# Optimization experiments

Hardware: AMD Instinct MI355X
Metric: run time of the kernel (lower is better)

## Reference

```python
import jax, jax.numpy as jnp
import numpy as np
from jax import lax

DSTATE, DINPUT, DMLP1, DMLP2, TRAJ = 64, 4, 256, 256, 8
BATCH, SEQ = 1024, 64


def setup_inputs() -> dict:
    key = jax.random.key(0)
    ks = jax.random.split(key, 4)
    f32 = jnp.float32
    return {
        "quat_seq": jax.random.normal(ks[0], (BATCH, SEQ, DINPUT), f32),
        "W1": jax.random.normal(ks[1], (DSTATE + DINPUT, DMLP1), f32) / np.sqrt(DSTATE + DINPUT),
        "b1": jnp.zeros((DMLP1,), f32),
        "W2": jax.random.normal(ks[2], (DMLP1, DMLP2), f32) / np.sqrt(DMLP1),
        "b2": jnp.zeros((DMLP2,), f32),
        "W3": jax.random.normal(ks[3], (DMLP2, DSTATE), f32) / np.sqrt(DMLP2),
        "b3": jnp.zeros((DSTATE,), f32),
    }


def reference(quat_seq, W1, b1, W2, b2, W3, b3):
    dt = 1.0 / (TRAJ - 1)  # uniform linspace(0,1,TRAJ) step

    def odefunc(h, q):
        # 3-layer tanh MLP on concat([h, q]); time-independent
        x = jnp.concatenate([h, q], axis=-1)          # [B, dstate+dinput]
        h1 = jnp.tanh(x @ W1 + b1)
        h2 = jnp.tanh(h1 @ W2 + b2)
        return h2 @ W3 + b3                            # [B, dstate]

    @jax.checkpoint
    def rk4_step(h, q):
        # torchdiffeq 'rk4' uses the 3/8-rule variant (rk4_alt_step_func)
        k1 = odefunc(h, q)
        k2 = odefunc(h + dt * k1 / 3.0, q)
        k3 = odefunc(h + dt * (k2 - k1 / 3.0), q)
        k4 = odefunc(h + dt * (k1 - k2 + k3), q)
        return h + dt * (k1 + 3.0 * (k2 + k3) + k4) / 8.0

    def per_token(h, q):
        # integrate over t_span, recording TRAJ states (including initial h)
        def body(hc, _):
            hn = rk4_step(hc, q)
            return hn, hn
        h_last, tail = lax.scan(body, h, None, length=TRAJ - 1)
        h_traj = jnp.concatenate([h[None], tail], axis=0)  # [TRAJ, B, dstate]
        return h_last, h_traj

    B = quat_seq.shape[0]
    h0 = jnp.zeros((B, DSTATE), quat_seq.dtype).at[:, 0].set(1.0)
    qs = jnp.swapaxes(quat_seq, 0, 1)  # [seq, B, dinput]
    h_final, trajs = lax.scan(per_token, h0, qs)  # trajs: [seq, TRAJ, B, dstate]
    trajectories = jnp.transpose(trajs, (2, 0, 1, 3))  # [B, seq, TRAJ, dstate]
    return h_final, trajectories
```

## Files before the change

kernel.cpp:

```cpp
#include <hip/hip_runtime.h>
#include <math.h>

#define NTHR 512
#define BT 4

__device__ __forceinline__ float fast_tanh(float x) {
    float ax = fabsf(x);
    float e  = __expf(-2.0f * ax);
    float r  = (1.0f - e) * __builtin_amdgcn_rcpf(1.0f + e);
    return copysignf(r, x);
}

__global__ __launch_bounds__(NTHR, 2)
void odernn_kernel(const float* __restrict__ quat,
                   const float* __restrict__ W1,
                   const float* __restrict__ b1,
                   const float* __restrict__ W2,
                   const float* __restrict__ b2,
                   const float* __restrict__ W3,
                   const float* __restrict__ b3,
                   float* __restrict__ out)
{
    __shared__ __align__(16) float sRed[8192];
    __shared__ __align__(16) float sH1[4][256];
    __shared__ __align__(16) float sH2[4][256];
    __shared__ __align__(16) float sC1[4][256];
    __shared__ __align__(16) float sY[4][64];

    const int t = threadIdx.x;
    const int w = t >> 6;
    const int l = t & 63;
    const int b0 = blockIdx.x * BT;

    const int j1a = t >> 1;
    const int kha = (t & 1) * 32;
    const int kb2 = w * 32;
    const int j1c = t & 255;
    const int bc  = (t >> 8) * 2;
    const int u3  = t & 15;
    const int ks3 = t >> 4;
    const int kb3 = ks3 * 8;
    const int rb = w;
    const int rj = l;

    float w1r[32];
    #pragma unroll
    for (int k = 0; k < 32; ++k) w1r[k] = W1[(kha + k) * 256 + j1a];

    float w2r[128];
    const float4* __restrict__ W2v4 = (const float4*)W2;
    #pragma unroll
    for (int k = 0; k < 32; ++k) {
        float4 v = W2v4[(size_t)(kb2 + k) * 64 + l];
        w2r[k * 4 + 0] = v.x; w2r[k * 4 + 1] = v.y;
        w2r[k * 4 + 2] = v.z; w2r[k * 4 + 3] = v.w;
    }
    float w3r[32];
    #pragma unroll
    for (int k = 0; k < 8; ++k) {
        float4 v = *(const float4*)&W3[(kb3 + k) * 64 + u3 * 4];
        w3r[k * 4 + 0] = v.x; w3r[k * 4 + 1] = v.y;
        w3r[k * 4 + 2] = v.z; w3r[k * 4 + 3] = v.w;
    }
    float w1q[4];
    #pragma unroll
    for (int m = 0; m < 4; ++m) w1q[m] = W1[(64 + m) * 256 + j1c];

    const float rb1  = b1[j1c];
    const float rb2c = b2[j1c];
    const float rb3e = b3[rj];

    float rH  = (rj == 0) ? 1.0f : 0.0f;
    float rk1 = 0.0f, rk2 = 0.0f, rk3 = 0.0f;
    if (t < 256) sY[rb][rj] = rH;

    const float dt = 1.0f / 7.0f;
    float* __restrict__ traj = out + 1024 * 64;

    for (int s = 0; s < 64; ++s) {
        if (t < 256) {
            float4 q0 = *(const float4*)&quat[((size_t)(b0 + 0) * 64 + s) * 4];
            float4 q1 = *(const float4*)&quat[((size_t)(b0 + 1) * 64 + s) * 4];
            float4 q2 = *(const float4*)&quat[((size_t)(b0 + 2) * 64 + s) * 4];
            float4 q3 = *(const float4*)&quat[((size_t)(b0 + 3) * 64 + s) * 4];
            sC1[0][t] = fmaf(q0.x, w1q[0], fmaf(q0.y, w1q[1], fmaf(q0.z, w1q[2], fmaf(q0.w, w1q[3], rb1))));
            sC1[1][t] = fmaf(q1.x, w1q[0], fmaf(q1.y, w1q[1], fmaf(q1.z, w1q[2], fmaf(q1.w, w1q[3], rb1))));
            sC1[2][t] = fmaf(q2.x, w1q[0], fmaf(q2.y, w1q[1], fmaf(q2.z, w1q[2], fmaf(q2.w, w1q[3], rb1))));
            sC1[3][t] = fmaf(q3.x, w1q[0], fmaf(q3.y, w1q[1], fmaf(q3.z, w1q[2], fmaf(q3.w, w1q[3], rb1))));
            traj[(((size_t)(b0 + rb) * 64 + s) * 8 + 0) * 64 + rj] = rH;
        }
        __syncthreads();

        for (int step = 1; step < 8; ++step) {
            #pragma unroll
            for (int mode = 1; mode <= 4; ++mode) {
                {
                    float a0 = 0.0f, a1 = 0.0f, a2 = 0.0f, a3 = 0.0f;
                    const float4* y4 = (const float4*)&sY[0][0];
                    const int yb = (t & 1) * 8;
                    #pragma unroll
                    for (int k4 = 0; k4 < 8; ++k4) {
                        float4 y0 = y4[0 * 16 + yb + k4];
                        float4 y1 = y4[1 * 16 + yb + k4];
                        float4 y2 = y4[2 * 16 + yb + k4];
                        float4 y3 = y4[3 * 16 + yb + k4];
                        #pragma unroll
                        for (int r = 0; r < 4; ++r) {
                            float wv = w1r[k4 * 4 + r];
                            a0 = fmaf(((const float*)&y0)[r], wv, a0);
                            a1 = fmaf(((const float*)&y1)[r], wv, a1);
                            a2 = fmaf(((const float*)&y2)[r], wv, a2);
                            a3 = fmaf(((const float*)&y3)[r], wv, a3);
                        }
                    }
                    a0 += __shfl_xor(a0, 1);
                    a1 += __shfl_xor(a1, 1);
                    a2 += __shfl_xor(a2, 1);
                    a3 += __shfl_xor(a3, 1);
                    const int bw = (t & 1) * 2;
                    float vA = (t & 1) ? a2 : a0;
                    float vB = (t & 1) ? a3 : a1;
                    sH1[bw][j1a]     = fast_tanh(vA + sC1[bw][j1a]);
                    sH1[bw + 1][j1a] = fast_tanh(vB + sC1[bw + 1][j1a]);
                }
                __syncthreads();
                {
                    float acc[4][4];
                    #pragma unroll
                    for (int bb = 0; bb < 4; ++bb)
                        #pragma unroll
                        for (int jj = 0; jj < 4; ++jj) acc[bb][jj] = 0.0f;
                    #pragma unroll
                    for (int k4 = 0; k4 < 8; ++k4) {
                        const int k = kb2 + k4 * 4;
                        float4 h0 = *(const float4*)&sH1[0][k];
                        float4 h1v = *(const float4*)&sH1[1][k];
                        float4 h2v = *(const float4*)&sH1[2][k];
                        float4 h3v = *(const float4*)&sH1[3][k];
                        #pragma unroll
                        for (int r = 0; r < 4; ++r) {
                            const int wi = (k4 * 4 + r) * 4;
                            float f0 = ((const float*)&h0)[r];
                            float f1 = ((const float*)&h1v)[r];
                            float f2 = ((const float*)&h2v)[r];
                            float f3 = ((const float*)&h3v)[r];
                            #pragma unroll
                            for (int jj = 0; jj < 4; ++jj) {
                                acc[0][jj] = fmaf(f0, w2r[wi + jj], acc[0][jj]);
                                acc[1][jj] = fmaf(f1, w2r[wi + jj], acc[1][jj]);
                                acc[2][jj] = fmaf(f2, w2r[wi + jj], acc[2][jj]);
                                acc[3][jj] = fmaf(f3, w2r[wi + jj], acc[3][jj]);
                            }
                        }
                    }
                    #pragma unroll
                    for (int bb = 0; bb < 4; ++bb)
                        *(float4*)&sRed[w * 1024 + bb * 256 + l * 4] =
                            make_float4(acc[bb][0], acc[bb][1], acc[bb][2], acc[bb][3]);
                }
                __syncthreads();
                {
                    float v0 = rb2c, v1 = 0.0f, u0 = rb2c, u1 = 0.0f;
                    #pragma unroll
                    for (int ks = 0; ks < 8; ks += 2) {
                        v0 += sRed[ks * 1024 + bc * 256 + j1c];
                        u0 += sRed[ks * 1024 + (bc + 1) * 256 + j1c];
                        v1 += sRed[(ks + 1) * 1024 + bc * 256 + j1c];
                        u1 += sRed[(ks + 1) * 1024 + (bc + 1) * 256 + j1c];
                    }
                    sH2[bc][j1c]     = fast_tanh(v0 + v1);
                    sH2[bc + 1][j1c] = fast_tanh(u0 + u1);
                }
                __syncthreads();
                {
                    float acc[4][4];
                    #pragma unroll
                    for (int bb = 0; bb < 4; ++bb)
                        #pragma unroll
                        for (int jj = 0; jj < 4; ++jj) acc[bb][jj] = 0.0f;
                    #pragma unroll
                    for (int k4 = 0; k4 < 2; ++k4) {
                        const int k = kb3 + k4 * 4;
                        float4 h0 = *(const float4*)&sH2[0][k];
                        float4 h1v = *(const float4*)&sH2[1][k];
                        float4 h2v = *(const float4*)&sH2[2][k];
                        float4 h3v = *(const float4*)&sH2[3][k];
                        #pragma unroll
                        for (int r = 0; r < 4; ++r) {
                            const int wi = (k4 * 4 + r) * 4;
                            float f0 = ((const float*)&h0)[r];
                            float f1 = ((const float*)&h1v)[r];
                            float f2 = ((const float*)&h2v)[r];
                            float f3 = ((const float*)&h3v)[r];
                            #pragma unroll
                            for (int jj = 0; jj < 4; ++jj) {
                                acc[0][jj] = fmaf(f0, w3r[wi + jj], acc[0][jj]);
                                acc[1][jj] = fmaf(f1, w3r[wi + jj], acc[1][jj]);
                                acc[2][jj] = fmaf(f2, w3r[wi + jj], acc[2][jj]);
                                acc[3][jj] = fmaf(f3, w3r[wi + jj], acc[3][jj]);
                            }
                        }
                    }
                    #pragma unroll
                    for (int bb = 0; bb < 4; ++bb)
                        *(float4*)&sRed[ks3 * 256 + bb * 64 + u3 * 4] =
                            make_float4(acc[bb][0], acc[bb][1], acc[bb][2], acc[bb][3]);
                }
                __syncthreads();
                if (t < 256) {
                    float s0 = rb3e, s1 = 0.0f, s2 = 0.0f, s3 = 0.0f;
                    #pragma unroll
                    for (int ks = 0; ks < 32; ks += 4) {
                        s0 += sRed[(ks + 0) * 256 + rb * 64 + rj];
                        s1 += sRed[(ks + 1) * 256 + rb * 64 + rj];
                        s2 += sRed[(ks + 2) * 256 + rb * 64 + rj];
                        s3 += sRed[(ks + 3) * 256 + rb * 64 + rj];
                    }
                    float k = (s0 + s1) + (s2 + s3);
                    float ynew;
                    if (mode == 1) {
                        rk1 = k;
                        ynew = fmaf(dt * (1.0f / 3.0f), rk1, rH);
                    } else if (mode == 2) {
                        rk2 = k;
                        ynew = fmaf(dt, rk2 - rk1 * (1.0f / 3.0f), rH);
                    } else if (mode == 3) {
                        rk3 = k;
                        ynew = fmaf(dt, rk1 - rk2 + rk3, rH);
                    } else {
                        rH = fmaf(dt * 0.125f, rk1 + 3.0f * (rk2 + rk3) + k, rH);
                        ynew = rH;
                        traj[(((size_t)(b0 + rb) * 64 + s) * 8 + step) * 64 + rj] = rH;
                    }
                    sY[rb][rj] = ynew;
                }
                __syncthreads();
            }
        }
    }
    if (t < 256) out[(size_t)(b0 + rb) * 64 + rj] = rH;
}

extern "C" void kernel_launch(void* const* d_in, const int* in_sizes, int n_in,
                              void* d_out, int out_size, void* d_ws, size_t ws_size,
                              hipStream_t stream) {
    const float* quat = (const float*)d_in[0];
    const float* W1   = (const float*)d_in[1];
    const float* b1   = (const float*)d_in[2];
    const float* W2   = (const float*)d_in[3];
    const float* b2   = (const float*)d_in[4];
    const float* W3   = (const float*)d_in[5];
    const float* b3   = (const float*)d_in[6];
    float* out = (float*)d_out;

    odernn_kernel<<<1024 / BT, NTHR, 0, stream>>>(quat, W1, b1, W2, b2, W3, b3, out);
}
```

Measured before the change: 5.657 ms.

## Replace shared-memory split-K reductions with in-wave shuffle reductions

Layers 2 and 3 change their work split so that the K-slices for each output column live in lanes of the same wavefront. The partial sums are then reduced with xor-shuffles instead of being written to a shared-memory scratch buffer and summed after an extra barrier. This removes the 32 KB sRed buffer and two __syncthreads per RK stage. The layer-1 q-projection weights are now reloaded from global memory every token to free registers. K-offsets are rotated per lane to avoid LDS bank conflicts. The cost is many more shuffle instructions and some duplicated work across lanes.

```diff
diff --git a/kernel.cpp b/kernel.cpp
--- a/kernel.cpp
+++ b/kernel.cpp
@@ -21,7 +21,6 @@
                    const float* __restrict__ b3,
                    float* __restrict__ out)
 {
-    __shared__ __align__(16) float sRed[8192];
     __shared__ __align__(16) float sH1[4][256];
     __shared__ __align__(16) float sH2[4][256];
     __shared__ __align__(16) float sC1[4][256];
@@ -33,62 +32,79 @@
     const int b0 = blockIdx.x * BT;
 
     const int j1a = t >> 1;
-    const int kha = (t & 1) * 32;
-    const int kb2 = w * 32;
-    const int j1c = t & 255;
-    const int bc  = (t >> 8) * 2;
-    const int u3  = t & 15;
-    const int ks3 = t >> 4;
-    const int kb3 = ks3 * 8;
-    const int rb = w;
-    const int rj = l;
+    const int bw  = (t & 1) * 2;
+    const int yb  = (t & 1) * 8;
+    const int ks2 = l & 7;
+    const int u2  = (w << 3) | (l >> 3);
+    const int kb2 = ks2 * 32;
+    const int bB  = l & 3;
+    const int jj0 = (l >> 2) & 1;
+    const int jB0 = u2 * 4 + jj0;
+    const int jB1 = u2 * 4 + jj0 + 2;
+    const int ks3  = l & 15;
+    const int jp3  = (w << 2) | (l >> 4);
+    const int kb3  = ks3 * 16;
+    const int rot3 = (l >> 1) & 3;
+    const int bD = (l >> 1) & 3;
+    const int jD = jp3 * 2 + (l & 1);
+    const bool ownD = (l & 8) == 0;
 
     float w1r[32];
     #pragma unroll
-    for (int k = 0; k < 32; ++k) w1r[k] = W1[(kha + k) * 256 + j1a];
+    for (int k = 0; k < 32; ++k) w1r[k] = W1[((t & 1) * 32 + k) * 256 + j1a];
 
     float w2r[128];
-    const float4* __restrict__ W2v4 = (const float4*)W2;
     #pragma unroll
-    for (int k = 0; k < 32; ++k) {
-        float4 v = W2v4[(size_t)(kb2 + k) * 64 + l];
-        w2r[k * 4 + 0] = v.x; w2r[k * 4 + 1] = v.y;
-        w2r[k * 4 + 2] = v.z; w2r[k * 4 + 3] = v.w;
+    for (int k4 = 0; k4 < 8; ++k4) {
+        const int ke = (k4 + ks2) & 7;
+        #pragma unroll
+        for (int r = 0; r < 4; ++r) {
+            float4 v = *(const float4*)&W2[(size_t)(kb2 + ke * 4 + r) * 256 + u2 * 4];
+            w2r[(k4 * 4 + r) * 4 + 0] = v.x;
+            w2r[(k4 * 4 + r) * 4 + 1] = v.y;
+            w2r[(k4 * 4 + r) * 4 + 2] = v.z;
+            w2r[(k4 * 4 + r) * 4 + 3] = v.w;
+        }
     }
     float w3r[32];
     #pragma unroll
-    for (int k = 0; k < 8; ++k) {
-        float4 v = *(const float4*)&W3[(kb3 + k) * 64 + u3 * 4];
-        w3r[k * 4 + 0] = v.x; w3r[k * 4 + 1] = v.y;
-        w3r[k * 4 + 2] = v.z; w3r[k * 4 + 3] = v.w;
+    for (int k4 = 0; k4 < 4; ++k4) {
+        const int ke = (k4 + rot3) & 3;
+        #pragma unroll
+        for (int r = 0; r < 4; ++r) {
+            float2 v = *(const float2*)&W3[(kb3 + ke * 4 + r) * 64 + jp3 * 2];
+            w3r[(k4 * 4 + r) * 2 + 0] = v.x;
+            w3r[(k4 * 4 + r) * 2 + 1] = v.y;
+        }
     }
-    float w1q[4];
-    #pragma unroll
-    for (int m = 0; m < 4; ++m) w1q[m] = W1[(64 + m) * 256 + j1c];
-
-    const float rb1  = b1[j1c];
-    const float rb2c = b2[j1c];
-    const float rb3e = b3[rj];
-
-    float rH  = (rj == 0) ? 1.0f : 0.0f;
+    const float rb2_0 = b2[jB0];
+    const float rb2_1 = b2[jB1];
+    const float rb3   = b3[jD];
+
+    float rH  = (jD == 0) ? 1.0f : 0.0f;
     float rk1 = 0.0f, rk2 = 0.0f, rk3 = 0.0f;
-    if (t < 256) sY[rb][rj] = rH;
+    if (ownD) sY[bD][jD] = rH;
 
     const float dt = 1.0f / 7.0f;
     float* __restrict__ traj = out + 1024 * 64;
 
     for (int s = 0; s < 64; ++s) {
         if (t < 256) {
+            float w1q0 = W1[64 * 256 + t];
+            float w1q1 = W1[65 * 256 + t];
+            float w1q2 = W1[66 * 256 + t];
+            float w1q3 = W1[67 * 256 + t];
+            float bb1  = b1[t];
             float4 q0 = *(const float4*)&quat[((size_t)(b0 + 0) * 64 + s) * 4];
             float4 q1 = *(const float4*)&quat[((size_t)(b0 + 1) * 64 + s) * 4];
             float4 q2 = *(const float4*)&quat[((size_t)(b0 + 2) * 64 + s) * 4];
             float4 q3 = *(const float4*)&quat[((size_t)(b0 + 3) * 64 + s) * 4];
-            sC1[0][t] = fmaf(q0.x, w1q[0], fmaf(q0.y, w1q[1], fmaf(q0.z, w1q[2], fmaf(q0.w, w1q[3], rb1))));
-            sC1[1][t] = fmaf(q1.x, w1q[0], fmaf(q1.y, w1q[1], fmaf(q1.z, w1q[2], fmaf(q1.w, w1q[3], rb1))));
-            sC1[2][t] = fmaf(q2.x, w1q[0], fmaf(q2.y, w1q[1], fmaf(q2.z, w1q[2], fmaf(q2.w, w1q[3], rb1))));
-            sC1[3][t] = fmaf(q3.x, w1q[0], fmaf(q3.y, w1q[1], fmaf(q3.z, w1q[2], fmaf(q3.w, w1q[3], rb1))));
-            traj[(((size_t)(b0 + rb) * 64 + s) * 8 + 0) * 64 + rj] = rH;
-        }
+            sC1[0][t] = fmaf(q0.x, w1q0, fmaf(q0.y, w1q1, fmaf(q0.z, w1q2, fmaf(q0.w, w1q3, bb1))));
+            sC1[1][t] = fmaf(q1.x, w1q0, fmaf(q1.y, w1q1, fmaf(q1.z, w1q2, fmaf(q1.w, w1q3, bb1))));
+            sC1[2][t] = fmaf(q2.x, w1q0, fmaf(q2.y, w1q1, fmaf(q2.z, w1q2, fmaf(q2.w, w1q3, bb1))));
+            sC1[3][t] = fmaf(q3.x, w1q0, fmaf(q3.y, w1q1, fmaf(q3.z, w1q2, fmaf(q3.w, w1q3, bb1))));
+        }
+        if (ownD) traj[(((size_t)(b0 + bD) * 64 + s) * 8 + 0) * 64 + jD] = rH;
         __syncthreads();
 
         for (int step = 1; step < 8; ++step) {
@@ -97,7 +113,6 @@
                 {
                     float a0 = 0.0f, a1 = 0.0f, a2 = 0.0f, a3 = 0.0f;
                     const float4* y4 = (const float4*)&sY[0][0];
-                    const int yb = (t & 1) * 8;
                     #pragma unroll
                     for (int k4 = 0; k4 < 8; ++k4) {
                         float4 y0 = y4[0 * 16 + yb + k4];
@@ -117,7 +132,6 @@
                     a1 += __shfl_xor(a1, 1);
                     a2 += __shfl_xor(a2, 1);
                     a3 += __shfl_xor(a3, 1);
-                    const int bw = (t & 1) * 2;
                     float vA = (t & 1) ? a2 : a0;
                     float vB = (t & 1) ? a3 : a1;
                     sH1[bw][j1a]     = fast_tanh(vA + sC1[bw][j1a]);
@@ -132,113 +146,101 @@
                         for (int jj = 0; jj < 4; ++jj) acc[bb][jj] = 0.0f;
                     #pragma unroll
                     for (int k4 = 0; k4 < 8; ++k4) {
-                        const int k = kb2 + k4 * 4;
-                        float4 h0 = *(const float4*)&sH1[0][k];
-                        float4 h1v = *(const float4*)&sH1[1][k];
-                        float4 h2v = *(const float4*)&sH1[2][k];
-                        float4 h3v = *(const float4*)&sH1[3][k];
-                        #pragma unroll
-                        for (int r = 0; r < 4; ++r) {
-                            const int wi = (k4 * 4 + r) * 4;
-                            float f0 = ((const float*)&h0)[r];
-                            float f1 = ((const float*)&h1v)[r];
-                            float f2 = ((const float*)&h2v)[r];
-                            float f3 = ((const float*)&h3v)[r];
+                        const int ka = kb2 + ((k4 + ks2) & 7) * 4;
+                        #pragma unroll
+                        for (int bb = 0; bb < 4; ++bb) {
+                            float4 h = *(const float4*)&sH1[bb][ka];
                             #pragma unroll
-                            for (int jj = 0; jj < 4; ++jj) {
-                                acc[0][jj] = fmaf(f0, w2r[wi + jj], acc[0][jj]);
-                                acc[1][jj] = fmaf(f1, w2r[wi + jj], acc[1][jj]);
-                                acc[2][jj] = fmaf(f2, w2r[wi + jj], acc[2][jj]);
-                                acc[3][jj] = fmaf(f3, w2r[wi + jj], acc[3][jj]);
+                            for (int r = 0; r < 4; ++r) {
+                                const int wi = (k4 * 4 + r) * 4;
+                                float f = ((const float*)&h)[r];
+                                acc[bb][0] = fmaf(f, w2r[wi + 0], acc[bb][0]);
+                                acc[bb][1] = fmaf(f, w2r[wi + 1], acc[bb][1]);
+                                acc[bb][2] = fmaf(f, w2r[wi + 2], acc[bb][2]);
+                                acc[bb][3] = fmaf(f, w2r[wi + 3], acc[bb][3]);
                             }
                         }
                     }
                     #pragma unroll
-                    for (int bb = 0; bb < 4; ++bb)
-                        *(float4*)&sRed[w * 1024 + bb * 256 + l * 4] =
-                            make_float4(acc[bb][0], acc[bb][1], acc[bb][2], acc[bb][3]);
+                    for (int m = 1; m <= 4; m <<= 1)
+                        #pragma unroll
+                        for (int bb = 0; bb < 4; ++bb)
+                            #pragma unroll
+                            for (int jj = 0; jj < 4; ++jj)
+                                acc[bb][jj] += __shfl_xor(acc[bb][jj], m);
+                    float z0 = (l & 4) ? acc[0][1] : acc[0][0];
+                    float z1 = (l & 4) ? acc[1][1] : acc[1][0];
+                    float z2 = (l & 4) ? acc[2][1] : acc[2][0];
+                    float z3 = (l & 4) ? acc[3][1] : acc[3][0];
+                    float y0 = (l & 1) ? z1 : z0;
+                    float y1 = (l & 1) ? z3 : z2;
+                    float o0 = (l & 2) ? y1 : y0;
+                    z0 = (l & 4) ? acc[0][3] : acc[0][2];
+                    z1 = (l & 4) ? acc[1][3] : acc[1][2];
+                    z2 = (l & 4) ? acc[2][3] : acc[2][2];
+                    z3 = (l & 4) ? acc[3][3] : acc[3][2];
+                    y0 = (l & 1) ? z1 : z0;
+                    y1 = (l & 1) ? z3 : z2;
+                    float o1 = (l & 2) ? y1 : y0;
+                    sH2[bB][jB0] = fast_tanh(o0 + rb2_0);
+                    sH2[bB][jB1] = fast_tanh(o1 + rb2_1);
                 }
                 __syncthreads();
                 {
-                    float v0 = rb2c, v1 = 0.0f, u0 = rb2c, u1 = 0.0f;
-                    #pragma unroll
-                    for (int ks = 0; ks < 8; ks += 2) {
-                        v0 += sRed[ks * 1024 + bc * 256 + j1c];
-                        u0 += sRed[ks * 1024 + (bc + 1) * 256 + j1c];
-                        v1 += sRed[(ks + 1) * 1024 + bc * 256 + j1c];
-                        u1 += sRed[(ks + 1) * 1024 + (bc + 1) * 256 + j1c];
-                    }
-                    sH2[bc][j1c]     = fast_tanh(v0 + v1);
-                    sH2[bc + 1][j1c] = fast_tanh(u0 + u1);
-                }
-                __syncthreads();
-                {
-                    float acc[4][4];
-                    #pragma unroll
-                    for (int bb = 0; bb < 4; ++bb)
-                        #pragma unroll
-                        for (int jj = 0; jj < 4; ++jj) acc[bb][jj] = 0.0f;
-                    #pragma unroll
-                    for (int k4 = 0; k4 < 2; ++k4) {
-                        const int k = kb3 + k4 * 4;
-                        float4 h0 = *(const float4*)&sH2[0][k];
-                        float4 h1v = *(const float4*)&sH2[1][k];
-                        float4 h2v = *(const float4*)&sH2[2][k];
-                        float4 h3v = *(const float4*)&sH2[3][k];
-                        #pragma unroll
-                        for (int r = 0; r < 4; ++r) {
-                            const int wi = (k4 * 4 + r) * 4;
-                            float f0 = ((const float*)&h0)[r];
-                            float f1 = ((const float*)&h1v)[r];
-                            float f2 = ((const float*)&h2v)[r];
-                            float f3 = ((const float*)&h3v)[r];
+                    float acc[4][2];
+                    #pragma unroll
+                    for (int bb = 0; bb < 4; ++bb) { acc[bb][0] = 0.0f; acc[bb][1] = 0.0f; }
+                    #pragma unroll
+                    for (int k4 = 0; k4 < 4; ++k4) {
+                        const int ka = kb3 + ((k4 + rot3) & 3) * 4;
+                        #pragma unroll
+                        for (int bb = 0; bb < 4; ++bb) {
+                            float4 h = *(const float4*)&sH2[bb][ka];
                             #pragma unroll
-                            for (int jj = 0; jj < 4; ++jj) {
-                                acc[0][jj] = fmaf(f0, w3r[wi + jj], acc[0][jj]);
-                                acc[1][jj] = fmaf(f1, w3r[wi + jj], acc[1][jj]);
-                                acc[2][jj] = fmaf(f2, w3r[wi + jj], acc[2][jj]);
-                                acc[3][jj] = fmaf(f3, w3r[wi + jj], acc[3][jj]);
+                            for (int r = 0; r < 4; ++r) {
+                                const int wi = (k4 * 4 + r) * 2;
+                                float f = ((const float*)&h)[r];
+                                acc[bb][0] = fmaf(f, w3r[wi + 0], acc[bb][0]);
+                                acc[bb][1] = fmaf(f, w3r[wi + 1], acc[bb][1]);
                             }
                         }
                     }
                     #pragma unroll
-                    for (int bb = 0; bb < 4; ++bb)
-                        *(float4*)&sRed[ks3 * 256 + bb * 64 + u3 * 4] =
-                            make_float4(acc[bb][0], acc[bb][1], acc[bb][2], acc[bb][3]);
-                }
-                __syncthreads();
-                if (t < 256) {
-                    float s0 = rb3e, s1 = 0.0f, s2 = 0.0f, s3 = 0.0f;
-                    #pragma unroll
-                    for (int ks = 0; ks < 32; ks += 4) {
-                        s0 += sRed[(ks + 0) * 256 + rb * 64 + rj];
-                        s1 += sRed[(ks + 1) * 256 + rb * 64 + rj];
-                        s2 += sRed[(ks + 2) * 256 + rb * 64 + rj];
-                        s3 += sRed[(ks + 3) * 256 + rb * 64 + rj];
-                    }
-                    float k = (s0 + s1) + (s2 + s3);
+                    for (int m = 1; m <= 8; m <<= 1)
+                        #pragma unroll
+                        for (int bb = 0; bb < 4; ++bb) {
+                            acc[bb][0] += __shfl_xor(acc[bb][0], m);
+                            acc[bb][1] += __shfl_xor(acc[bb][1], m);
+                        }
+                    float z0 = (l & 1) ? acc[0][1] : acc[0][0];
+                    float z1 = (l & 1) ? acc[1][1] : acc[1][0];
+                    float z2 = (l & 1) ? acc[2][1] : acc[2][0];
+                    float z3 = (l & 1) ? acc[3][1] : acc[3][0];
+                    float y0 = (l & 2) ? z1 : z0;
+                    float y1 = (l & 2) ? z3 : z2;
+                    float kk = ((l & 4) ? y1 : y0) + rb3;
                     float ynew;
                     if (mode == 1) {
-                        rk1 = k;
+                        rk1 = kk;
                         ynew = fmaf(dt * (1.0f / 3.0f), rk1, rH);
                     } else if (mode == 2) {
-                        rk2 = k;
+                        rk2 = kk;
                         ynew = fmaf(dt, rk2 - rk1 * (1.0f / 3.0f), rH);
                     } else if (mode == 3) {
-                        rk3 = k;
+                        rk3 = kk;
                         ynew = fmaf(dt, rk1 - rk2 + rk3, rH);
                     } else {
-                        rH = fmaf(dt * 0.125f, rk1 + 3.0f * (rk2 + rk3) + k, rH);
+                        rH = fmaf(dt * 0.125f, rk1 + 3.0f * (rk2 + rk3) + kk, rH);
                         ynew = rH;
-                        traj[(((size_t)(b0 + rb) * 64 + s) * 8 + step) * 64 + rj] = rH;
-                    }
-                    sY[rb][rj] = ynew;
+                        if (ownD) traj[(((size_t)(b0 + bD) * 64 + s) * 8 + step) * 64 + jD] = rH;
+                    }
+                    if (ownD) sY[bD][jD] = ynew;
                 }
                 __syncthreads();
             }
         }
     }
-    if (t < 256) out[(size_t)(b0 + rb) * 64 + rj] = rH;
+    if (ownD) out[(size_t)(b0 + bD) * 64 + jD] = rH;
 }
 
 extern "C" void kernel_launch(void* const* d_in, const int* in_sizes, int n_in,
```

After: 7.789 ms. 37.7% more time.

## Remap layer-1 and layer-3 work partitions with DPP quad reductions

Applied to the files above, without the earlier changes.

Layer 1 is remapped so each thread computes two output columns over a quarter of the K dimension, with partial sums combined by DPP quad adds instead of a shuffle. Layer 3 now reduces its K-split partials within each quad through DPP, then writes one XOR-swizzled float4 per lane. The final reduction reads 8 partials instead of 32. The aim is to cut LDS traffic and reduction latency on the serial RK4 critical path, at the cost of extra select instructions and DPP ops.

```diff
diff --git a/kernel.cpp b/kernel.cpp
--- a/kernel.cpp
+++ b/kernel.cpp
@@ -9,6 +9,12 @@
     float e  = __expf(-2.0f * ax);
     float r  = (1.0f - e) * __builtin_amdgcn_rcpf(1.0f + e);
     return copysignf(r, x);
+}
+
+template <int CTRL>
+__device__ __forceinline__ float dpp_add(float x) {
+    int yi = __builtin_amdgcn_update_dpp(0, __builtin_bit_cast(int, x), CTRL, 0xF, 0xF, true);
+    return x + __builtin_bit_cast(float, yi);
 }
 
 __global__ __launch_bounds__(NTHR, 2)
@@ -30,23 +36,27 @@
     const int t = threadIdx.x;
     const int w = t >> 6;
     const int l = t & 63;
+    const int q = l & 3;
     const int b0 = blockIdx.x * BT;
 
-    const int j1a = t >> 1;
-    const int kha = (t & 1) * 32;
+    const int ksa = l & 3;
+    const int j0  = (w * 16 + (l >> 2)) * 2;
     const int kb2 = w * 32;
     const int j1c = t & 255;
     const int bc  = (t >> 8) * 2;
-    const int u3  = t & 15;
-    const int ks3 = t >> 4;
-    const int kb3 = ks3 * 8;
-    const int rb = w;
+    const int ksd = (w << 2) | q;
+    const int kb3 = ksd * 8;
+    const int u3  = l >> 2;
+    const int j03 = u3 * 4;
+    const int rb = (t >> 6) & 3;
     const int rj = l;
 
     float w1r[32];
     #pragma unroll
-    for (int k = 0; k < 32; ++k) w1r[k] = W1[(kha + k) * 256 + j1a];
-
+    for (int k = 0; k < 16; ++k) {
+        float2 v = *(const float2*)&W1[(ksa * 16 + k) * 256 + j0];
+        w1r[k * 2 + 0] = v.x; w1r[k * 2 + 1] = v.y;
+    }
     float w2r[128];
     const float4* __restrict__ W2v4 = (const float4*)W2;
     #pragma unroll
@@ -58,7 +68,7 @@
     float w3r[32];
     #pragma unroll
     for (int k = 0; k < 8; ++k) {
-        float4 v = *(const float4*)&W3[(kb3 + k) * 64 + u3 * 4];
+        float4 v = *(const float4*)&W3[(kb3 + k) * 64 + j03];
         w3r[k * 4 + 0] = v.x; w3r[k * 4 + 1] = v.y;
         w3r[k * 4 + 2] = v.z; w3r[k * 4 + 3] = v.w;
     }
@@ -95,33 +105,47 @@
             #pragma unroll
             for (int mode = 1; mode <= 4; ++mode) {
                 {
-                    float a0 = 0.0f, a1 = 0.0f, a2 = 0.0f, a3 = 0.0f;
+                    float a[4][2];
+                    #pragma unroll
+                    for (int bb = 0; bb < 4; ++bb) { a[bb][0] = 0.0f; a[bb][1] = 0.0f; }
                     const float4* y4 = (const float4*)&sY[0][0];
-                    const int yb = (t & 1) * 8;
-                    #pragma unroll
-                    for (int k4 = 0; k4 < 8; ++k4) {
-                        float4 y0 = y4[0 * 16 + yb + k4];
-                        float4 y1 = y4[1 * 16 + yb + k4];
-                        float4 y2 = y4[2 * 16 + yb + k4];
-                        float4 y3 = y4[3 * 16 + yb + k4];
+                    #pragma unroll
+                    for (int kk = 0; kk < 4; ++kk) {
+                        float4 yv0 = y4[0 * 16 + ksa * 4 + kk];
+                        float4 yv1 = y4[1 * 16 + ksa * 4 + kk];
+                        float4 yv2 = y4[2 * 16 + ksa * 4 + kk];
+                        float4 yv3 = y4[3 * 16 + ksa * 4 + kk];
                         #pragma unroll
                         for (int r = 0; r < 4; ++r) {
-                            float wv = w1r[k4 * 4 + r];
-                            a0 = fmaf(((const float*)&y0)[r], wv, a0);
-                            a1 = fmaf(((const float*)&y1)[r], wv, a1);
-                            a2 = fmaf(((const float*)&y2)[r], wv, a2);
-                            a3 = fmaf(((const float*)&y3)[r], wv, a3);
-                        }
-                    }
-                    a0 += __shfl_xor(a0, 1);
-                    a1 += __shfl_xor(a1, 1);
-                    a2 += __shfl_xor(a2, 1);
-                    a3 += __shfl_xor(a3, 1);
-                    const int bw = (t & 1) * 2;
-                    float vA = (t & 1) ? a2 : a0;
-                    float vB = (t & 1) ? a3 : a1;
-                    sH1[bw][j1a]     = fast_tanh(vA + sC1[bw][j1a]);
-                    sH1[bw + 1][j1a] = fast_tanh(vB + sC1[bw + 1][j1a]);
+                            float w0 = w1r[(kk * 4 + r) * 2 + 0];
+                            float w1v = w1r[(kk * 4 + r) * 2 + 1];
+                            float f0 = ((const float*)&yv0)[r];
+                            float f1 = ((const float*)&yv1)[r];
+                            float f2 = ((const float*)&yv2)[r];
+                            float f3 = ((const float*)&yv3)[r];
+                            a[0][0] = fmaf(f0, w0, a[0][0]); a[0][1] = fmaf(f0, w1v, a[0][1]);
+                            a[1][0] = fmaf(f1, w0, a[1][0]); a[1][1] = fmaf(f1, w1v, a[1][1]);
+                            a[2][0] = fmaf(f2, w0, a[2][0]); a[2][1] = fmaf(f2, w1v, a[2][1]);
+                            a[3][0] = fmaf(f3, w0, a[3][0]); a[3][1] = fmaf(f3, w1v, a[3][1]);
+                        }
+                    }
+                    #pragma unroll
+                    for (int bb = 0; bb < 4; ++bb) {
+                        #pragma unroll
+                        for (int jj = 0; jj < 2; ++jj) {
+                            a[bb][jj] = dpp_add<0xB1>(a[bb][jj]);
+                            a[bb][jj] = dpp_add<0x4E>(a[bb][jj]);
+                        }
+                    }
+                    float z0 = (l & 1) ? a[1][0] : a[0][0];
+                    float z1 = (l & 1) ? a[3][0] : a[2][0];
+                    float o0 = (l & 2) ? z1 : z0;
+                    z0 = (l & 1) ? a[1][1] : a[0][1];
+                    z1 = (l & 1) ? a[3][1] : a[2][1];
+                    float o1 = (l & 2) ? z1 : z0;
+                    float2 c = *(const float2*)&sC1[q][j0];
+                    float2 h = make_float2(fast_tanh(o0 + c.x), fast_tanh(o1 + c.y));
+                    *(float2*)&sH1[q][j0] = h;
                 }
                 __syncthreads();
                 {
@@ -179,15 +203,15 @@
                         #pragma unroll
                         for (int jj = 0; jj < 4; ++jj) acc[bb][jj] = 0.0f;
                     #pragma unroll
-                    for (int k4 = 0; k4 < 2; ++k4) {
-                        const int k = kb3 + k4 * 4;
+                    for (int kk = 0; kk < 2; ++kk) {
+                        const int k = kb3 + kk * 4;
                         float4 h0 = *(const float4*)&sH2[0][k];
                         float4 h1v = *(const float4*)&sH2[1][k];
                         float4 h2v = *(const float4*)&sH2[2][k];
                         float4 h3v = *(const float4*)&sH2[3][k];
                         #pragma unroll
                         for (int r = 0; r < 4; ++r) {
-                            const int wi = (k4 * 4 + r) * 4;
+                            const int wi = (kk * 4 + r) * 4;
                             float f0 = ((const float*)&h0)[r];
                             float f1 = ((const float*)&h1v)[r];
                             float f2 = ((const float*)&h2v)[r];
@@ -203,18 +227,38 @@
                     }
                     #pragma unroll
                     for (int bb = 0; bb < 4; ++bb)
-                        *(float4*)&sRed[ks3 * 256 + bb * 64 + u3 * 4] =
-                            make_float4(acc[bb][0], acc[bb][1], acc[bb][2], acc[bb][3]);
+                        #pragma unroll
+                        for (int jj = 0; jj < 4; ++jj) {
+                            acc[bb][jj] = dpp_add<0xB1>(acc[bb][jj]);
+                            acc[bb][jj] = dpp_add<0x4E>(acc[bb][jj]);
+                        }
+                    float o0, o1, o2, o3;
+                    {
+                        float z0 = (l & 1) ? acc[1][0] : acc[0][0];
+                        float z1 = (l & 1) ? acc[3][0] : acc[2][0];
+                        o0 = (l & 2) ? z1 : z0;
+                        z0 = (l & 1) ? acc[1][1] : acc[0][1];
+                        z1 = (l & 1) ? acc[3][1] : acc[2][1];
+                        o1 = (l & 2) ? z1 : z0;
+                        z0 = (l & 1) ? acc[1][2] : acc[0][2];
+                        z1 = (l & 1) ? acc[3][2] : acc[2][2];
+                        o2 = (l & 2) ? z1 : z0;
+                        z0 = (l & 1) ? acc[1][3] : acc[0][3];
+                        z1 = (l & 1) ? acc[3][3] : acc[2][3];
+                        o3 = (l & 2) ? z1 : z0;
+                    }
+                    ((float4*)sRed)[w * 64 + q * 16 + (u3 ^ q)] = make_float4(o0, o1, o2, o3);
                 }
                 __syncthreads();
                 if (t < 256) {
+                    const int jb = rb * 64 + (((rj >> 2) ^ rb) * 4) + (rj & 3);
                     float s0 = rb3e, s1 = 0.0f, s2 = 0.0f, s3 = 0.0f;
                     #pragma unroll
-                    for (int ks = 0; ks < 32; ks += 4) {
-                        s0 += sRed[(ks + 0) * 256 + rb * 64 + rj];
-                        s1 += sRed[(ks + 1) * 256 + rb * 64 + rj];
-                        s2 += sRed[(ks + 2) * 256 + rb * 64 + rj];
-                        s3 += sRed[(ks + 3) * 256 + rb * 64 + rj];
+                    for (int wk = 0; wk < 8; wk += 4) {
+                        s0 += sRed[(wk + 0) * 256 + jb];
+                        s1 += sRed[(wk + 1) * 256 + jb];
+                        s2 += sRed[(wk + 2) * 256 + jb];
+                        s3 += sRed[(wk + 3) * 256 + jb];
                     }
                     float k = (s0 + s1) + (s2 + s3);
                     float ynew;
```

New measurement: 5.598 ms. Within noise of the previous version (-1.0%).
